# Optimization experiments

Measured on AMD Instinct MI355X. Metric: run time of the kernel, lower is better.

## Reference

```python
import jax, jax.numpy as jnp
import numpy as np

N = 10000      # nodes
E = 160000     # edges (avg degree 16)
H = 128        # hidden_dim
L = 4          # propagation_depth
G = 64         # graphs in batch
ATOM_V = 119
BOND_V = 5
AVG_D_LOG = 1.0
EPS_SCALE = 1e-8


def setup_inputs() -> dict:
    key = jax.random.key(0)
    ks = jax.random.split(key, 12)
    x = jax.random.randint(ks[0], (N,), 0, ATOM_V)
    edge_index = jax.random.randint(ks[1], (2, E), 0, N)
    edge_attr = jax.random.randint(ks[2], (E,), 0, BOND_V)
    batch = jnp.sort(jax.random.randint(ks[3], (N,), 0, G))
    atom_emb = jax.random.normal(ks[4], (ATOM_V, H), jnp.float32) * 0.1
    bond_emb = jax.random.normal(ks[5], (BOND_V, H), jnp.float32) * 0.1
    pre_W = jax.random.normal(ks[6], (L, 3 * H, H), jnp.float32) / np.sqrt(3 * H)
    pre_b = jnp.zeros((L, H), jnp.float32)
    post_W = jax.random.normal(ks[7], (L, 10 * H, H), jnp.float32) / np.sqrt(10 * H)
    post_b = jnp.zeros((L, H), jnp.float32)
    out_W1 = jax.random.normal(ks[8], (3 * H, H), jnp.float32) / np.sqrt(3 * H)
    out_b1 = jnp.zeros((H,), jnp.float32)
    out_W2 = jax.random.normal(ks[9], (H, 1), jnp.float32) / np.sqrt(H)
    out_b2 = jnp.zeros((1,), jnp.float32)
    return {"x": x, "edge_index": edge_index, "edge_attr": edge_attr, "batch": batch,
            "atom_emb": atom_emb, "bond_emb": bond_emb,
            "pre_W": pre_W, "pre_b": pre_b, "post_W": post_W, "post_b": post_b,
            "out_W1": out_W1, "out_b1": out_b1, "out_W2": out_W2, "out_b2": out_b2}


def _seg_mean_sum_max(v, idx, num_seg, cnt):
    s = jax.ops.segment_sum(v, idx, num_segments=num_seg)
    mean = s / jnp.maximum(cnt, 1.0)[:, None]
    mx = jax.ops.segment_max(v, idx, num_segments=num_seg)
    mx = jnp.where(cnt[:, None] > 0, mx, 0.0)  # empty segments -> 0 (torch scatter)
    return mean, s, mx


def _clean(a):
    return jnp.where(jnp.isnan(a) | jnp.isinf(a), 0.0, a)


def reference(x, edge_index, edge_attr, batch, atom_emb, bond_emb,
              pre_W, pre_b, post_W, post_b, out_W1, out_b1, out_W2, out_b2):
    h = atom_emb[x]            # [N, H] atom encoder
    e = bond_emb[edge_attr]    # [E, H] bond encoder
    row, col = edge_index[0], edge_index[1]
    n = h.shape[0]
    deg = jax.ops.segment_sum(jnp.ones_like(col, jnp.float32), col, num_segments=n)
    D = deg[:, None]
    logD = jnp.log(D + 1.0)
    amp_fac = logD / AVG_D_LOG                       # amplification scaler
    att_fac = AVG_D_LOG / jnp.maximum(logD, EPS_SCALE)  # attenuation scaler
    n_layers = pre_W.shape[0]
    for l in range(n_layers):
        h_in = h
        z2 = jnp.concatenate([h[row], h[col], e], axis=-1)         # [E, 3H]
        msg = z2 @ pre_W[l] + pre_b[l]                             # pretrans (1 layer, no act)
        mean, s, mx = _seg_mean_sum_max(msg, col, n, deg)
        hagg = jnp.concatenate([mean, s, mx], axis=-1)             # [N, 3H]
        hcat = jnp.concatenate([hagg, hagg * amp_fac, hagg * att_fac, h_in], axis=-1)  # [N, 10H]
        h = hcat @ post_W[l] + post_b[l]                           # posttrans (1 layer)
        h = h + h_in                                               # residual
    # readout over graphs
    cnt = jax.ops.segment_sum(jnp.ones((n,), jnp.float32), batch, num_segments=G)
    rmean, rsum, rmax = _seg_mean_sum_max(h, batch, G, cnt)
    r = _clean(jnp.concatenate([rmean, rsum, rmax], axis=-1))      # [G, 3H]
    out = jax.nn.relu(r @ out_W1 + out_b1) @ out_W2 + out_b2       # [G, 1]
    return _clean(out)
```

## Files before the change

kernel.cpp:

```cpp
#include <hip/hip_runtime.h>
#include <hip/hip_bf16.h>
#include <math.h>

#define NN 10000
#define NE 160000
#define HD 128
#define NL 4
#define NG 64

typedef __attribute__((ext_vector_type(8))) short bf16x8;
typedef __attribute__((ext_vector_type(4))) short bf16x4;
typedef __attribute__((ext_vector_type(4))) float f32x4;

static __device__ __forceinline__ short f2bf(float f) {
    unsigned u = __float_as_uint(f);
    unsigned r = (u + 0x7FFFu + ((u >> 16) & 1u)) >> 16;
    return (short)r;
}
static __device__ __forceinline__ float bf2f(short s) {
    return __uint_as_float(((unsigned)(unsigned short)s) << 16);
}

__global__ void embed_kernel(const int* __restrict__ x, const float* __restrict__ atom_emb,
                             float* __restrict__ h, float* __restrict__ deg,
                             int* __restrict__ cursor) {
    int idx = blockIdx.x * 256 + threadIdx.x;
    if (idx < NN) { deg[idx] = 0.f; cursor[idx] = 0; }
    if (idx < NN * HD) {
        int n = idx >> 7, f = idx & 127;
        h[idx] = atom_emb[x[n] * HD + f];
    }
}

__global__ void deg_kernel(const int* __restrict__ col, float* __restrict__ deg) {
    int e = blockIdx.x * 256 + threadIdx.x;
    if (e < NE) atomicAdd(&deg[col[e]], 1.f);
}

__global__ __launch_bounds__(1024) void scan_facs_kernel(const float* __restrict__ deg,
                                                         int* __restrict__ offsets,
                                                         float* __restrict__ amp,
                                                         float* __restrict__ att) {
    __shared__ int s[1024];
    int t = threadIdx.x;
    int base = t * 10;
    int v[10];
    int lsum = 0;
    #pragma unroll
    for (int i = 0; i < 10; ++i) {
        int idx = base + i;
        int d = (idx < NN) ? (int)deg[idx] : 0;
        v[i] = d;
        lsum += d;
        if (idx < NN) {
            float logD = logf((float)d + 1.f);
            amp[idx] = logD;
            att[idx] = 1.f / fmaxf(logD, 1e-8f);
        }
    }
    s[t] = lsum;
    __syncthreads();
    for (int off = 1; off < 1024; off <<= 1) {
        int x2 = (t >= off) ? s[t - off] : 0;
        __syncthreads();
        s[t] += x2;
        __syncthreads();
    }
    int run = s[t] - lsum;
    #pragma unroll
    for (int i = 0; i < 10; ++i) {
        int idx = base + i;
        if (idx < NN) offsets[idx] = run;
        run += v[i];
    }
    if (t == 1023) offsets[NN] = run;
}

__global__ void scatter_kernel(const int* __restrict__ row, const int* __restrict__ col,
                               const int* __restrict__ ea, const int* __restrict__ offsets,
                               int* __restrict__ cursor, int* __restrict__ perm) {
    int e = blockIdx.x * 256 + threadIdx.x;
    if (e < NE) {
        int c = col[e];
        int pos = offsets[c] + atomicAdd(&cursor[c], 1);
        perm[pos] = row[e] | (ea[e] << 14);
    }
}

__global__ __launch_bounds__(256) void convw_bondtab_kernel(
    const float* __restrict__ bond_emb,
    const float* __restrict__ pre_W, const float* __restrict__ pre_b,
    const float* __restrict__ post_W,
    float* __restrict__ btab, short* __restrict__ pre_Wt, short* __restrict__ post_Wt) {
    int b = blockIdx.x;
    if (b < 20) {
        if (threadIdx.x < 128) {
            int l = b / 5, bb = b % 5;
            int f = threadIdx.x;
            const float* W2 = pre_W + (size_t)l * 384 * HD + 256 * HD;
            const float* eb = bond_emb + bb * HD;
            float acc = pre_b[l * HD + f];
            for (int k = 0; k < HD; ++k) acc = fmaf(eb[k], W2[k * HD + f], acc);
            btab[(l * 5 + bb) * HD + f] = acc;
        }
        return;
    }
    int idx = (b - 20) * 256 + threadIdx.x;
    if (idx < NL * 4 * 256 * 32) {
        int l = idx >> 15;
        int r = idx & 32767;
        int kblk = r >> 13;
        int rr = r & 8191;
        int j = rr >> 5, k = rr & 31;
        const float* Wl = pre_W + (size_t)l * 384 * HD;
        float v = (j < 128) ? Wl[(kblk * 32 + k) * HD + j]
                            : Wl[(128 + kblk * 32 + k) * HD + (j - 128)];
        pre_Wt[idx] = f2bf(v);
    }
    if (idx < NL * 40 * 128 * 32) {
        int l = idx / 163840;
        int r = idx % 163840;
        int kblk = r >> 12;
        int rr = r & 4095;
        int j = rr >> 5, k = rr & 31;
        post_Wt[idx] = f2bf(post_W[(size_t)l * 163840 + (size_t)(kblk * 32 + k) * HD + j]);
    }
}

__global__ __launch_bounds__(256) void pre_gemm_mfma(const float* __restrict__ h,
                                                     const short* __restrict__ Wt,
                                                     short* __restrict__ hw0,
                                                     float* __restrict__ hw1) {
    __shared__ short Ap[16][136];
    int t = threadIdx.x;
    int nb = blockIdx.x * 16;
    {
        int nl = t >> 4, f = (t & 15) * 8;
        int n = nb + nl;
        const float* src = h + (size_t)n * HD + f;
        float4 x0 = *(const float4*)src, x1 = *(const float4*)(src + 4);
        bf16x8 pk;
        pk[0]=f2bf(x0.x); pk[1]=f2bf(x0.y); pk[2]=f2bf(x0.z); pk[3]=f2bf(x0.w);
        pk[4]=f2bf(x1.x); pk[5]=f2bf(x1.y); pk[6]=f2bf(x1.z); pk[7]=f2bf(x1.w);
        *(bf16x8*)&Ap[nl][f] = pk;
    }
    __syncthreads();
    int wave = t >> 6, lane = t & 63;
    int lx = lane & 15, kb = lane >> 4;
    f32x4 acc[4];
    #pragma unroll
    for (int j = 0; j < 4; ++j) acc[j] = (f32x4){0.f, 0.f, 0.f, 0.f};

    for (int ks = 0; ks < 4; ++ks) {
        bf16x8 a = *(const bf16x8*)&Ap[lx][ks * 32 + kb * 8];
        const short* bp = Wt + (size_t)ks * 8192 + (size_t)(wave * 64 + lx) * 32 + kb * 8;
        #pragma unroll
        for (int jj = 0; jj < 4; ++jj) {
            bf16x8 bfr = *(const bf16x8*)(bp + jj * 512);
            acc[jj] = __builtin_amdgcn_mfma_f32_16x16x32_bf16(a, bfr, acc[jj], 0, 0, 0);
        }
    }
    #pragma unroll
    for (int jj = 0; jj < 4; ++jj) {
        int c = wave * 64 + jj * 16 + lx;
        #pragma unroll
        for (int r_ = 0; r_ < 4; ++r_) {
            int n2 = nb + kb * 4 + r_;
            if (c < 128) hw0[(size_t)n2 * HD + c] = f2bf(acc[jj][r_]);
            else         hw1[(size_t)n2 * HD + (c - 128)] = acc[jj][r_];
        }
    }
}

__global__ __launch_bounds__(256) void agg_node_gemm_mfma(
    const short* __restrict__ hw0, const float* __restrict__ hw1,
    const float* __restrict__ btab,
    const int* __restrict__ offsets, const int* __restrict__ perm,
    const float* __restrict__ hin,
    const float* __restrict__ amp, const float* __restrict__ att,
    const short* __restrict__ Wt , const float* __restrict__ bias,
    float* __restrict__ hout) {
    __shared__ short Ap[16][1288];
    __shared__ float btab_s[5][128];
    int t = threadIdx.x;
    int nb = blockIdx.x * 16;

    if (t < 160) {
        int b = t >> 5, f4 = (t & 31) * 4;
        *(f32x4*)&btab_s[b][f4] = *(const f32x4*)(btab + b * HD + f4);
    }
    __syncthreads();

    {
        int nl = t >> 4;
        int n = nb + nl;
        int f = (t & 15) * 8;
        int s0 = offsets[n];
        int d = offsets[n + 1] - s0;
        f32x4 sum0 = {0.f,0.f,0.f,0.f}, sum1 = {0.f,0.f,0.f,0.f};
        f32x4 mx0 = {-INFINITY,-INFINITY,-INFINITY,-INFINITY};
        f32x4 mx1 = mx0;
        int i = 0;
        for (; i + 2 <= d; i += 2) {
            int p0 = perm[s0 + i], p1 = perm[s0 + i + 1];
            bf16x8 a0 = *(const bf16x8*)(hw0 + (size_t)(p0 & 16383) * HD + f);
            bf16x8 a1 = *(const bf16x8*)(hw0 + (size_t)(p1 & 16383) * HD + f);
            const float* t0 = &btab_s[p0 >> 14][f];
            const float* t1 = &btab_s[p1 >> 14][f];
            f32x4 b00 = *(const f32x4*)t0, b01 = *(const f32x4*)(t0 + 4);
            f32x4 b10 = *(const f32x4*)t1, b11 = *(const f32x4*)(t1 + 4);
            f32x4 v00, v01, v10, v11;
            #pragma unroll
            for (int q = 0; q < 4; ++q) {
                v00[q] = bf2f(a0[q]) + b00[q];
                v01[q] = bf2f(a0[q + 4]) + b01[q];
                v10[q] = bf2f(a1[q]) + b10[q];
                v11[q] = bf2f(a1[q + 4]) + b11[q];
            }
            sum0 += v00 + v10; sum1 += v01 + v11;
            #pragma unroll
            for (int q = 0; q < 4; ++q) {
                mx0[q] = fmaxf(mx0[q], fmaxf(v00[q], v10[q]));
                mx1[q] = fmaxf(mx1[q], fmaxf(v01[q], v11[q]));
            }
        }
        if (i < d) {
            int p0 = perm[s0 + i];
            bf16x8 a0 = *(const bf16x8*)(hw0 + (size_t)(p0 & 16383) * HD + f);
            const float* t0 = &btab_s[p0 >> 14][f];
            f32x4 b00 = *(const f32x4*)t0, b01 = *(const f32x4*)(t0 + 4);
            f32x4 v00, v01;
            #pragma unroll
            for (int q = 0; q < 4; ++q) {
                v00[q] = bf2f(a0[q]) + b00[q];
                v01[q] = bf2f(a0[q + 4]) + b01[q];
            }
            sum0 += v00; sum1 += v01;
            #pragma unroll
            for (int q = 0; q < 4; ++q) {
                mx0[q] = fmaxf(mx0[q], v00[q]);
                mx1[q] = fmaxf(mx1[q], v01[q]);
            }
        }
        const float* cp = hw1 + (size_t)n * HD + f;
        f32x4 c0 = *(const f32x4*)cp, c1 = *(const f32x4*)(cp + 4);
        f32x4 me0, me1, so0, so1, mo0, mo1;
        if (d > 0) {
            float df = (float)d, di = 1.f / df;
            so0 = sum0 + df * c0;  so1 = sum1 + df * c1;
            me0 = sum0 * di + c0;  me1 = sum1 * di + c1;
            mo0 = mx0 + c0;        mo1 = mx1 + c1;
        } else {
            me0 = (f32x4){0.f,0.f,0.f,0.f}; me1 = me0;
            so0 = me0; so1 = me0; mo0 = me0; mo1 = me0;
        }
        float f_amp = amp[n], f_att = att[n];
        #pragma unroll
        for (int fi = 0; fi < 3; ++fi) {
            float fac = (fi == 0) ? 1.f : ((fi == 1) ? f_amp : f_att);
            #pragma unroll
            for (int ag = 0; ag < 3; ++ag) {
                f32x4 r0 = (ag == 0) ? me0 : ((ag == 1) ? so0 : mo0);
                f32x4 r1 = (ag == 0) ? me1 : ((ag == 1) ? so1 : mo1);
                bf16x8 pk;
                #pragma unroll
                for (int q = 0; q < 4; ++q) {
                    pk[q]     = f2bf(r0[q] * fac);
                    pk[q + 4] = f2bf(r1[q] * fac);
                }
                *(bf16x8*)&Ap[nl][(fi * 3 + ag) * 128 + f] = pk;
            }
        }
        {
            const float* src = hin + (size_t)n * HD + f;
            float4 x0 = *(const float4*)src, x1 = *(const float4*)(src + 4);
            bf16x8 pk;
            pk[0]=f2bf(x0.x); pk[1]=f2bf(x0.y); pk[2]=f2bf(x0.z); pk[3]=f2bf(x0.w);
            pk[4]=f2bf(x1.x); pk[5]=f2bf(x1.y); pk[6]=f2bf(x1.z); pk[7]=f2bf(x1.w);
            *(bf16x8*)&Ap[nl][9 * 128 + f] = pk;
        }
    }
    __syncthreads();

    int wave = t >> 6, lane = t & 63;
    int lx = lane & 15, kb = lane >> 4;
    f32x4 acc0 = {0.f,0.f,0.f,0.f}, acc1 = acc0;
    for (int ks = 0; ks < 40; ++ks) {
        bf16x8 a = *(const bf16x8*)&Ap[lx][ks * 32 + kb * 8];
        const short* bp = Wt + (size_t)ks * 4096 + (size_t)(wave * 32 + lx) * 32 + kb * 8;
        bf16x8 b0 = *(const bf16x8*)bp;
        bf16x8 b1 = *(const bf16x8*)(bp + 512);
        acc0 = __builtin_amdgcn_mfma_f32_16x16x32_bf16(a, b0, acc0, 0, 0, 0);
        acc1 = __builtin_amdgcn_mfma_f32_16x16x32_bf16(a, b1, acc1, 0, 0, 0);
    }
    #pragma unroll
    for (int jj = 0; jj < 2; ++jj) {
        int c = wave * 32 + jj * 16 + lx;
        float bc = bias[c];
        f32x4 av = jj ? acc1 : acc0;
        #pragma unroll
        for (int r_ = 0; r_ < 4; ++r_) {
            int n2 = nb + kb * 4 + r_;
            size_t off = (size_t)n2 * HD + c;
            hout[off] = av[r_] + bc + hin[off];
        }
    }
}

__global__ __launch_bounds__(256) void pool_out_kernel(
    const float* __restrict__ h, const int* __restrict__ batch,
    const float* __restrict__ W1, const float* __restrict__ b1,
    const float* __restrict__ W2, const float* __restrict__ b2,
    float* __restrict__ out)
{
    __shared__ float rs[384];
    __shared__ float red[256];
    __shared__ float s2[128], m2[128];
    int g = blockIdx.x, t = threadIdx.x;
    int lo = 0, hi = NN;
    while (lo < hi) { int mid = (lo + hi) >> 1; if (batch[mid] < g) lo = mid + 1; else hi = mid; }
    int lo2 = lo, hi2 = NN;
    while (lo2 < hi2) { int mid = (lo2 + hi2) >> 1; if (batch[mid] < g + 1) lo2 = mid + 1; else hi2 = mid; }
    int cnt = lo2 - lo;
    int f = t & 127, grp = t >> 7;
    float sum = 0.f, mx = -INFINITY;
    for (int n = lo + grp; n < lo2; n += 2) {
        float v = h[(size_t)n * HD + f];
        sum += v; mx = fmaxf(mx, v);
    }
    if (grp == 1) { s2[f] = sum; m2[f] = mx; }
    __syncthreads();
    if (grp == 0) {
        sum += s2[f]; mx = fmaxf(mx, m2[f]);
        float mean = (cnt > 0) ? sum / (float)cnt : 0.f;
        float so = (cnt > 0) ? sum : 0.f;
        float mo = (cnt > 0) ? mx : 0.f;
        if (isnan(mean) || isinf(mean)) mean = 0.f;
        if (isnan(so) || isinf(so)) so = 0.f;
        if (isnan(mo) || isinf(mo)) mo = 0.f;
        rs[f] = mean; rs[128 + f] = so; rs[256 + f] = mo;
    }
    __syncthreads();
    {
        int j = t & 127, kh = t >> 7;
        float acc = 0.f;
        for (int k = kh * 192; k < kh * 192 + 192; ++k)
            acc = fmaf(rs[k], W1[k * HD + j], acc);
        red[t] = acc;
    }
    __syncthreads();
    if (t < 128) {
        float v = fmaxf(red[t] + red[128 + t] + b1[t], 0.f);
        red[t] = v * W2[t];
    }
    __syncthreads();
    for (int s = 64; s > 0; s >>= 1) {
        if (t < s) red[t] += red[t + s];
        __syncthreads();
    }
    if (t == 0) {
        float o = red[0] + b2[0];
        if (isnan(o) || isinf(o)) o = 0.f;
        out[g] = o;
    }
}

extern "C" void kernel_launch(void* const* d_in, const int* in_sizes, int n_in,
                              void* d_out, int out_size, void* d_ws, size_t ws_size,
                              hipStream_t stream)
{
    const int* x          = (const int*)d_in[0];
    const int* ei         = (const int*)d_in[1];
    const int* ea         = (const int*)d_in[2];
    const int* batch      = (const int*)d_in[3];
    const float* atom_emb = (const float*)d_in[4];
    const float* bond_emb = (const float*)d_in[5];
    const float* pre_W    = (const float*)d_in[6];
    const float* pre_b    = (const float*)d_in[7];
    const float* post_W   = (const float*)d_in[8];
    const float* post_b   = (const float*)d_in[9];
    const float* out_W1   = (const float*)d_in[10];
    const float* out_b1   = (const float*)d_in[11];
    const float* out_W2   = (const float*)d_in[12];
    const float* out_b2   = (const float*)d_in[13];
    float* out = (float*)d_out;
    const int* row = ei;
    const int* col = ei + NE;

    char* p = (char*)d_ws;
    auto alloc = [&](size_t bytes) { char* r = p; p += (bytes + 255) & ~(size_t)255; return r; };
    float*    deg     = (float*)alloc((size_t)NN * 4);
    float*    amp     = (float*)alloc((size_t)NN * 4);
    float*    att     = (float*)alloc((size_t)NN * 4);
    int*      offsets = (int*)alloc((size_t)(NN + 1) * 4);
    int*      cursor  = (int*)alloc((size_t)NN * 4);
    int*      perm    = (int*)alloc((size_t)NE * 4);
    float*    hA      = (float*)alloc((size_t)NN * HD * 4);
    float*    hB      = (float*)alloc((size_t)NN * HD * 4);
    short*    hw0     = (short*)alloc((size_t)NN * HD * 2);
    float*    hw1     = (float*)alloc((size_t)NN * HD * 4);
    float*    btab    = (float*)alloc((size_t)NL * 5 * HD * 4);
    short*    pre_Wt  = (short*)alloc((size_t)NL * 4 * 256 * 32 * 2);
    short*    post_Wt = (short*)alloc((size_t)NL * 40 * 128 * 32 * 2);

    embed_kernel<<<(NN * HD) / 256, 256, 0, stream>>>(x, atom_emb, hA, deg, cursor);
    deg_kernel<<<(NE + 255) / 256, 256, 0, stream>>>(col, deg);
    scan_facs_kernel<<<1, 1024, 0, stream>>>(deg, offsets, amp, att);
    scatter_kernel<<<(NE + 255) / 256, 256, 0, stream>>>(row, col, ea, offsets, cursor, perm);
    convw_bondtab_kernel<<<20 + (NL * 40 * 128 * 32 + 255) / 256, 256, 0, stream>>>(
        bond_emb, pre_W, pre_b, post_W, btab, pre_Wt, post_Wt);

    float* curH = hA;
    float* nxtH = hB;
    for (int l = 0; l < NL; ++l) {
        pre_gemm_mfma<<<NN / 16, 256, 0, stream>>>(
            curH, pre_Wt + (size_t)l * 4 * 256 * 32, hw0, hw1);
        agg_node_gemm_mfma<<<NN / 16, 256, 0, stream>>>(
            hw0, hw1, btab + (size_t)l * 5 * HD, offsets, perm,
            curH, amp, att, post_Wt + (size_t)l * 40 * 128 * 32,
            post_b + (size_t)l * HD, nxtH);
        float* tmp = curH; curH = nxtH; nxtH = tmp;
    }

    pool_out_kernel<<<NG, 256, 0, stream>>>(curH, batch, out_W1, out_b1, out_W2, out_b2, out);
}
```

Measured before the change: 299.6 us.

## Fuse next-layer pre-GEMM into aggregation kernel and merge setup kernels

The per-node pretrans GEMM for layer l+1 now runs inside the layer-l aggregation/posttrans kernel. The new h tile is converted to bf16 in shared memory and multiplied by the next layer's pre-weights, with ping-pong hw buffers. Separately, the degree-count atomics are merged into the weight-conversion setup kernel, cutting launch count. This removes three pre_gemm launches and the re-read of h from global memory, at the cost of more shared memory and registers in the fused kernel, which may lower occupancy.

```diff
diff --git a/kernel.cpp b/kernel.cpp
--- a/kernel.cpp
+++ b/kernel.cpp
@@ -21,9 +21,9 @@
     return __uint_as_float(((unsigned)(unsigned short)s) << 16);
 }
 
-__global__ void embed_kernel(const int* __restrict__ x, const float* __restrict__ atom_emb,
-                             float* __restrict__ h, float* __restrict__ deg,
-                             int* __restrict__ cursor) {
+__global__ void setup1_kernel(const int* __restrict__ x, const float* __restrict__ atom_emb,
+                              float* __restrict__ h, float* __restrict__ deg,
+                              int* __restrict__ cursor) {
     int idx = blockIdx.x * 256 + threadIdx.x;
     if (idx < NN) { deg[idx] = 0.f; cursor[idx] = 0; }
     if (idx < NN * HD) {
@@ -32,70 +32,22 @@
     }
 }
 
-__global__ void deg_kernel(const int* __restrict__ col, float* __restrict__ deg) {
-    int e = blockIdx.x * 256 + threadIdx.x;
-    if (e < NE) atomicAdd(&deg[col[e]], 1.f);
-}
-
-__global__ __launch_bounds__(1024) void scan_facs_kernel(const float* __restrict__ deg,
-                                                         int* __restrict__ offsets,
-                                                         float* __restrict__ amp,
-                                                         float* __restrict__ att) {
-    __shared__ int s[1024];
-    int t = threadIdx.x;
-    int base = t * 10;
-    int v[10];
-    int lsum = 0;
-    #pragma unroll
-    for (int i = 0; i < 10; ++i) {
-        int idx = base + i;
-        int d = (idx < NN) ? (int)deg[idx] : 0;
-        v[i] = d;
-        lsum += d;
-        if (idx < NN) {
-            float logD = logf((float)d + 1.f);
-            amp[idx] = logD;
-            att[idx] = 1.f / fmaxf(logD, 1e-8f);
-        }
-    }
-    s[t] = lsum;
-    __syncthreads();
-    for (int off = 1; off < 1024; off <<= 1) {
-        int x2 = (t >= off) ? s[t - off] : 0;
-        __syncthreads();
-        s[t] += x2;
-        __syncthreads();
-    }
-    int run = s[t] - lsum;
-    #pragma unroll
-    for (int i = 0; i < 10; ++i) {
-        int idx = base + i;
-        if (idx < NN) offsets[idx] = run;
-        run += v[i];
-    }
-    if (t == 1023) offsets[NN] = run;
-}
-
-__global__ void scatter_kernel(const int* __restrict__ row, const int* __restrict__ col,
-                               const int* __restrict__ ea, const int* __restrict__ offsets,
-                               int* __restrict__ cursor, int* __restrict__ perm) {
-    int e = blockIdx.x * 256 + threadIdx.x;
-    if (e < NE) {
-        int c = col[e];
-        int pos = offsets[c] + atomicAdd(&cursor[c], 1);
-        perm[pos] = row[e] | (ea[e] << 14);
-    }
-}
-
-__global__ __launch_bounds__(256) void convw_bondtab_kernel(
+__global__ __launch_bounds__(256) void setup2_kernel(
+    const int* __restrict__ col, float* __restrict__ deg,
     const float* __restrict__ bond_emb,
     const float* __restrict__ pre_W, const float* __restrict__ pre_b,
     const float* __restrict__ post_W,
     float* __restrict__ btab, short* __restrict__ pre_Wt, short* __restrict__ post_Wt) {
     int b = blockIdx.x;
-    if (b < 20) {
+    if (b < 625) {
+        int e = b * 256 + threadIdx.x;
+        if (e < NE) atomicAdd(&deg[col[e]], 1.f);
+        return;
+    }
+    if (b < 645) {
+        int lb = b - 625;
         if (threadIdx.x < 128) {
-            int l = b / 5, bb = b % 5;
+            int l = lb / 5, bb = lb % 5;
             int f = threadIdx.x;
             const float* W2 = pre_W + (size_t)l * 384 * HD + 256 * HD;
             const float* eb = bond_emb + bb * HD;
@@ -105,7 +57,7 @@
         }
         return;
     }
-    int idx = (b - 20) * 256 + threadIdx.x;
+    int idx = (b - 645) * 256 + threadIdx.x;
     if (idx < NL * 4 * 256 * 32) {
         int l = idx >> 15;
         int r = idx & 32767;
@@ -124,6 +76,56 @@
         int rr = r & 4095;
         int j = rr >> 5, k = rr & 31;
         post_Wt[idx] = f2bf(post_W[(size_t)l * 163840 + (size_t)(kblk * 32 + k) * HD + j]);
+    }
+}
+
+__global__ __launch_bounds__(1024) void scan_facs_kernel(const float* __restrict__ deg,
+                                                         int* __restrict__ offsets,
+                                                         float* __restrict__ amp,
+                                                         float* __restrict__ att) {
+    __shared__ int s[1024];
+    int t = threadIdx.x;
+    int base = t * 10;
+    int v[10];
+    int lsum = 0;
+    #pragma unroll
+    for (int i = 0; i < 10; ++i) {
+        int idx = base + i;
+        int d = (idx < NN) ? (int)deg[idx] : 0;
+        v[i] = d;
+        lsum += d;
+        if (idx < NN) {
+            float logD = logf((float)d + 1.f);
+            amp[idx] = logD;
+            att[idx] = 1.f / fmaxf(logD, 1e-8f);
+        }
+    }
+    s[t] = lsum;
+    __syncthreads();
+    for (int off = 1; off < 1024; off <<= 1) {
+        int x2 = (t >= off) ? s[t - off] : 0;
+        __syncthreads();
+        s[t] += x2;
+        __syncthreads();
+    }
+    int run = s[t] - lsum;
+    #pragma unroll
+    for (int i = 0; i < 10; ++i) {
+        int idx = base + i;
+        if (idx < NN) offsets[idx] = run;
+        run += v[i];
+    }
+    if (t == 1023) offsets[NN] = run;
+}
+
+__global__ void scatter_kernel(const int* __restrict__ row, const int* __restrict__ col,
+                               const int* __restrict__ ea, const int* __restrict__ offsets,
+                               int* __restrict__ cursor, int* __restrict__ perm) {
+    int e = blockIdx.x * 256 + threadIdx.x;
+    if (e < NE) {
+        int c = col[e];
+        int pos = offsets[c] + atomicAdd(&cursor[c], 1);
+        perm[pos] = row[e] | (ea[e] << 14);
     }
 }
 
@@ -179,8 +181,11 @@
     const float* __restrict__ hin,
     const float* __restrict__ amp, const float* __restrict__ att,
     const short* __restrict__ Wt , const float* __restrict__ bias,
-    float* __restrict__ hout) {
+    float* __restrict__ hout,
+    const short* __restrict__ nextWt ,
+    short* __restrict__ hw0n, float* __restrict__ hw1n) {
     __shared__ short Ap[16][1288];
+    __shared__ short Ap2[16][136];
     __shared__ float btab_s[5][128];
     int t = threadIdx.x;
     int nb = blockIdx.x * 16;
@@ -302,7 +307,34 @@
         for (int r_ = 0; r_ < 4; ++r_) {
             int n2 = nb + kb * 4 + r_;
             size_t off = (size_t)n2 * HD + c;
-            hout[off] = av[r_] + bc + hin[off];
+            float ho = av[r_] + bc + hin[off];
+            hout[off] = ho;
+            Ap2[n2 - nb][c] = f2bf(ho);
+        }
+    }
+    if (nextWt == nullptr) return;
+    __syncthreads();
+
+    f32x4 acc[4];
+    #pragma unroll
+    for (int j = 0; j < 4; ++j) acc[j] = (f32x4){0.f, 0.f, 0.f, 0.f};
+    for (int ks = 0; ks < 4; ++ks) {
+        bf16x8 a = *(const bf16x8*)&Ap2[lx][ks * 32 + kb * 8];
+        const short* bp = nextWt + (size_t)ks * 8192 + (size_t)(wave * 64 + lx) * 32 + kb * 8;
+        #pragma unroll
+        for (int jj = 0; jj < 4; ++jj) {
+            bf16x8 bfr = *(const bf16x8*)(bp + jj * 512);
+            acc[jj] = __builtin_amdgcn_mfma_f32_16x16x32_bf16(a, bfr, acc[jj], 0, 0, 0);
+        }
+    }
+    #pragma unroll
+    for (int jj = 0; jj < 4; ++jj) {
+        int c = wave * 64 + jj * 16 + lx;
+        #pragma unroll
+        for (int r_ = 0; r_ < 4; ++r_) {
+            int n2 = nb + kb * 4 + r_;
+            if (c < 128) hw0n[(size_t)n2 * HD + c] = f2bf(acc[jj][r_]);
+            else         hw1n[(size_t)n2 * HD + (c - 128)] = acc[jj][r_];
         }
     }
 }
@@ -397,28 +429,34 @@
     int*      perm    = (int*)alloc((size_t)NE * 4);
     float*    hA      = (float*)alloc((size_t)NN * HD * 4);
     float*    hB      = (float*)alloc((size_t)NN * HD * 4);
-    short*    hw0     = (short*)alloc((size_t)NN * HD * 2);
-    float*    hw1     = (float*)alloc((size_t)NN * HD * 4);
+    short*    hw0A    = (short*)alloc((size_t)NN * HD * 2);
+    short*    hw0B    = (short*)alloc((size_t)NN * HD * 2);
+    float*    hw1A    = (float*)alloc((size_t)NN * HD * 4);
+    float*    hw1B    = (float*)alloc((size_t)NN * HD * 4);
     float*    btab    = (float*)alloc((size_t)NL * 5 * HD * 4);
     short*    pre_Wt  = (short*)alloc((size_t)NL * 4 * 256 * 32 * 2);
     short*    post_Wt = (short*)alloc((size_t)NL * 40 * 128 * 32 * 2);
 
-    embed_kernel<<<(NN * HD) / 256, 256, 0, stream>>>(x, atom_emb, hA, deg, cursor);
-    deg_kernel<<<(NE + 255) / 256, 256, 0, stream>>>(col, deg);
+    setup1_kernel<<<(NN * HD) / 256, 256, 0, stream>>>(x, atom_emb, hA, deg, cursor);
+    setup2_kernel<<<645 + (NL * 40 * 128 * 32 + 255) / 256, 256, 0, stream>>>(
+        col, deg, bond_emb, pre_W, pre_b, post_W, btab, pre_Wt, post_Wt);
     scan_facs_kernel<<<1, 1024, 0, stream>>>(deg, offsets, amp, att);
     scatter_kernel<<<(NE + 255) / 256, 256, 0, stream>>>(row, col, ea, offsets, cursor, perm);
-    convw_bondtab_kernel<<<20 + (NL * 40 * 128 * 32 + 255) / 256, 256, 0, stream>>>(
-        bond_emb, pre_W, pre_b, post_W, btab, pre_Wt, post_Wt);
+
+    pre_gemm_mfma<<<NN / 16, 256, 0, stream>>>(hA, pre_Wt, hw0A, hw1A);
 
     float* curH = hA;
     float* nxtH = hB;
     for (int l = 0; l < NL; ++l) {
-        pre_gemm_mfma<<<NN / 16, 256, 0, stream>>>(
-            curH, pre_Wt + (size_t)l * 4 * 256 * 32, hw0, hw1);
+        short* hw0_in  = (l & 1) ? hw0B : hw0A;
+        float* hw1_in  = (l & 1) ? hw1B : hw1A;
+        short* hw0_out = (l & 1) ? hw0A : hw0B;
+        float* hw1_out = (l & 1) ? hw1A : hw1B;
+        const short* nextWt = (l + 1 < NL) ? (pre_Wt + (size_t)(l + 1) * 4 * 256 * 32) : nullptr;
         agg_node_gemm_mfma<<<NN / 16, 256, 0, stream>>>(
-            hw0, hw1, btab + (size_t)l * 5 * HD, offsets, perm,
+            hw0_in, hw1_in, btab + (size_t)l * 5 * HD, offsets, perm,
             curH, amp, att, post_Wt + (size_t)l * 40 * 128 * 32,
-            post_b + (size_t)l * HD, nxtH);
+            post_b + (size_t)l * HD, nxtH, nextWt, hw0_out, hw1_out);
         float* tmp = curH; curH = nxtH; nxtH = tmp;
     }
 
```

Result: faster. 287.5 us (-4.0%).
